# Kernel optimization log

Hardware: AMD Instinct MI355X
Metric: run time of the kernel (lower is better)

Reference implementation:

```python
import jax, jax.numpy as jnp
import numpy as np

B, S, D = 1, 4096, 2048
H, KVH, HD = 16, 4, 128  # heads, kv heads, head_dim
ROPE_BASE = 10000.0


def _rope_cos_sin(position_ids):
    # inv_freq: [HD/2]
    inv_freq = 1.0 / (ROPE_BASE ** (jnp.arange(0, HD, 2, dtype=jnp.float32) / HD))
    # freqs: [B, S, HD/2] -> emb: [B, S, HD] (concat(freqs, freqs))
    freqs = position_ids.astype(jnp.float32)[..., None] * inv_freq
    emb = jnp.concatenate([freqs, freqs], axis=-1)
    # [B, 1, S, HD] to broadcast over heads
    return jnp.cos(emb)[:, None, :, :], jnp.sin(emb)[:, None, :, :]


def _rotate_half(x):
    x1, x2 = x[..., : HD // 2], x[..., HD // 2 :]
    return jnp.concatenate([-x2, x1], axis=-1)


def setup_inputs() -> dict:
    key = jax.random.key(0)
    ks = jax.random.split(key, 5)
    s = 0.02
    return {
        "hidden_states": jax.random.normal(ks[0], (B, S, D), jnp.float32),
        "Wq": jax.random.normal(ks[1], (H * HD, D), jnp.float32) * s,
        "Wk": jax.random.normal(ks[2], (KVH * HD, D), jnp.float32) * s,
        "Wv": jax.random.normal(ks[3], (KVH * HD, D), jnp.float32) * s,
        "Wo": jax.random.normal(ks[4], (D, H * HD), jnp.float32) * s,
        "position_ids": jnp.arange(S, dtype=jnp.int64 if jax.config.jax_enable_x64 else jnp.int32)[None, :].repeat(B, 0),
    }


def reference(hidden_states, Wq, Wk, Wv, Wo, position_ids):
    b, s, _ = hidden_states.shape
    # projections (no bias): [b, s, nheads*hd] -> [b, nh, s, hd]
    q = (hidden_states @ Wq.T).reshape(b, s, H, HD).transpose(0, 2, 1, 3)
    k = (hidden_states @ Wk.T).reshape(b, s, KVH, HD).transpose(0, 2, 1, 3)
    v = (hidden_states @ Wv.T).reshape(b, s, KVH, HD).transpose(0, 2, 1, 3)

    cos, sin = _rope_cos_sin(position_ids)  # [b,1,s,hd]
    q = q * cos + _rotate_half(q) * sin
    k = k * cos + _rotate_half(k) * sin

    # GQA: repeat kv heads (repeat_interleave along head dim)
    n_rep = H // KVH
    k = jnp.repeat(k, n_rep, axis=1)
    v = jnp.repeat(v, n_rep, axis=1)

    # eager quadratic attention with causal mask
    scores = jnp.einsum("bhqd,bhkd->bhqk", q, k) / jnp.sqrt(jnp.float32(HD))
    causal = jnp.tril(jnp.ones((s, s), dtype=bool))
    scores = jnp.where(causal[None, None], scores, jnp.finfo(scores.dtype).min)
    attn = jax.nn.softmax(scores, axis=-1)
    out = jnp.einsum("bhqk,bhkd->bhqd", attn, v)  # [b,h,s,hd]
    out = out.transpose(0, 2, 1, 3).reshape(b, s, H * HD)
    return out @ Wo.T
```

## Files before the change

### kernel.cpp

```cpp
#include <hip/hip_runtime.h>
#include <hip/hip_bf16.h>

constexpr int S   = 4096;
constexpr int D   = 2048;
constexpr int H   = 16;
constexpr int KVH = 4;
constexpr int HD  = 128;

using short8 = __attribute__((ext_vector_type(8))) short;
using f32x4  = __attribute__((ext_vector_type(4))) float;
using f32x16 = __attribute__((ext_vector_type(16))) float;

__device__ inline ushort f2bf(float f) {
  union { float f; unsigned u; } x{f};
  unsigned r = x.u + 0x7FFFu + ((x.u >> 16) & 1u);
  return (ushort)(r >> 16);
}
__device__ inline float bf2f(ushort h) {
  union { unsigned u; float f; } x{(unsigned)h << 16};
  return x.f;
}
__device__ inline unsigned pkbf(float a, float b) {
  union { float f; unsigned u; } xa{a}, xb{b};
  unsigned ra = xa.u + 0x7FFFu + ((xa.u >> 16) & 1u);
  unsigned rb = xb.u + 0x7FFFu + ((xb.u >> 16) & 1u);
#if __has_builtin(__builtin_amdgcn_perm)
  return __builtin_amdgcn_perm(rb, ra, 0x07060302u);
#else
  return (rb & 0xFFFF0000u) | (ra >> 16);
#endif
}
__device__ inline unsigned pkbf_t(float a, float b) {
  union { float f; unsigned u; } xa{a}, xb{b};
#if __has_builtin(__builtin_amdgcn_perm)
  return __builtin_amdgcn_perm(xb.u, xa.u, 0x07060302u);
#else
  return (xb.u & 0xFFFF0000u) | (xa.u >> 16);
#endif
}
__device__ inline float fast_exp2(float x) {
#if __has_builtin(__builtin_amdgcn_exp2f)
  return __builtin_amdgcn_exp2f(x);
#else
  return exp2f(x);
#endif
}

__device__ inline void async_copy16(const ushort* g, ushort* l) {
  __builtin_amdgcn_global_load_lds(
      (const __attribute__((address_space(1))) unsigned int*)g,
      (__attribute__((address_space(3))) unsigned int*)l, 16, 0, 0);
}

constexpr size_t N_HID = (size_t)S * D;
constexpr size_t N_WQ  = (size_t)(H * HD) * D;
constexpr size_t N_WKV = (size_t)(KVH * HD) * D;
constexpr size_t C1_ = N_HID;
constexpr size_t C2_ = C1_ + N_WQ;
constexpr size_t C3_ = C2_ + N_WKV;
constexpr size_t C4_ = C3_ + N_WKV;
constexpr size_t C5_ = C4_ + N_WQ;

__global__ void cvt_all_kernel(const float* __restrict__ hid, const float* __restrict__ wq,
                               const float* __restrict__ wk, const float* __restrict__ wv,
                               const float* __restrict__ wo, ushort* __restrict__ dst) {
  size_t i = (size_t)blockIdx.x * blockDim.x + threadIdx.x;
  size_t off = i * 4;
  if (off >= C5_) return;
  const float* src;
  if      (off < C1_) src = hid + off;
  else if (off < C2_) src = wq + (off - C1_);
  else if (off < C3_) src = wk + (off - C2_);
  else if (off < C4_) src = wv + (off - C3_);
  else                src = wo + (off - C4_);
  float4 f = *(const float4*)src;
  ushort4 o;
  o.x = f2bf(f.x); o.y = f2bf(f.y); o.z = f2bf(f.z); o.w = f2bf(f.w);
  *(ushort4*)&dst[off] = o;
}

template <int OUT_MODE>
__device__ __forceinline__ void gemm_tile(const ushort* __restrict__ A,
                                          const ushort* __restrict__ Bt,
                                          void* __restrict__ Cv,
                                          int M, int N, int K, int bxi, int byi,
                                          ushort* As, ushort* Bs) {
  const int bm = byi * 128;
  const int bn = bxi * 128;
  const int tid  = threadIdx.x;
  const int lane = tid & 63;
  const int w    = tid >> 6;
  const int wr = w >> 1, wc = w & 1;
  const int lm = lane & 15, quad = lane >> 4;

  f32x4 acc[4][4];
#pragma unroll
  for (int i = 0; i < 4; ++i)
#pragma unroll
    for (int j = 0; j < 4; ++j) acc[i][j] = (f32x4){0.f, 0.f, 0.f, 0.f};

  for (int k0 = 0; k0 < K; k0 += 32) {
#pragma unroll
    for (int j = 0; j < 2; ++j) {
      int idx = j * 256 + tid;
      int row = idx >> 2;
      int col = (idx & 3) * 8;
      int ubase = (j * 256 + w * 64) * 8;
      async_copy16(A + (size_t)(bm + row) * K + k0 + col, &As[ubase]);
      async_copy16(Bt + (size_t)(bn + row) * K + k0 + col, &Bs[ubase]);
    }
    __syncthreads();
    short8 af[4], bfr[4];
#pragma unroll
    for (int t = 0; t < 4; ++t) {
      af[t]  = *(const short8*)&As[(wr * 64 + t * 16 + lm) * 32 + quad * 8];
      bfr[t] = *(const short8*)&Bs[(wc * 64 + t * 16 + lm) * 32 + quad * 8];
    }
#pragma unroll
    for (int i = 0; i < 4; ++i)
#pragma unroll
      for (int j = 0; j < 4; ++j)
        acc[i][j] = __builtin_amdgcn_mfma_f32_16x16x32_bf16(af[i], bfr[j], acc[i][j], 0, 0, 0);
    __syncthreads();
  }

#pragma unroll
  for (int i = 0; i < 4; ++i)
#pragma unroll
    for (int j = 0; j < 4; ++j) {
      if (OUT_MODE == 2) {
        int col  = bn + wc * 64 + j * 16 + lm;
        int rowb = bm + wr * 64 + i * 16 + quad * 4;
        ushort4 o4;
        o4.x = f2bf(acc[i][j][0]); o4.y = f2bf(acc[i][j][1]);
        o4.z = f2bf(acc[i][j][2]); o4.w = f2bf(acc[i][j][3]);
        *(ushort4*)&((ushort*)Cv)[(size_t)col * M + rowb] = o4;
      } else {
#pragma unroll
        for (int r = 0; r < 4; ++r) {
          size_t row = bm + wr * 64 + i * 16 + quad * 4 + r;
          size_t col = bn + wc * 64 + j * 16 + lm;
          if (OUT_MODE == 1) ((ushort*)Cv)[row * N + col] = f2bf(acc[i][j][r]);
          else               ((float*)Cv)[row * N + col]  = acc[i][j][r];
        }
      }
    }
}

__global__ __launch_bounds__(256) void gemm_qkv_kernel(const ushort* __restrict__ hb,
                                                       const ushort* __restrict__ wq,
                                                       const ushort* __restrict__ wk,
                                                       const ushort* __restrict__ wv,
                                                       ushort* __restrict__ qb,
                                                       ushort* __restrict__ kb,
                                                       ushort* __restrict__ vtb) {
  __shared__ __align__(16) ushort As[128 * 32];
  __shared__ __align__(16) ushort Bs[128 * 32];
  int bid = blockIdx.x;
  if (bid < 512) {
    gemm_tile<1>(hb, wq, qb, S, H * HD, D, bid & 15, bid >> 4, As, Bs);
  } else if (bid < 640) {
    int b = bid - 512;
    gemm_tile<1>(hb, wk, kb, S, KVH * HD, D, b & 3, b >> 2, As, Bs);
  } else {
    int b = bid - 640;
    gemm_tile<2>(hb, wv, vtb, S, KVH * HD, D, b & 3, b >> 2, As, Bs);
  }
}

template <int OUT_MODE>
__global__ __launch_bounds__(256) void gemm_bt_kernel(const ushort* __restrict__ A,
                                                      const ushort* __restrict__ Bt,
                                                      void* __restrict__ Cv,
                                                      int M, int N, int K) {
  __shared__ __align__(16) ushort As[128 * 32];
  __shared__ __align__(16) ushort Bs[128 * 32];
  gemm_tile<OUT_MODE>(A, Bt, Cv, M, N, K, blockIdx.x, blockIdx.y, As, Bs);
}

__global__ void rope_bf16_kernel(ushort* __restrict__ qb, ushort* __restrict__ kb,
                                 const int* __restrict__ pos_ids) {
  int idx = blockIdx.x * blockDim.x + threadIdx.x;
  const int total = S * (H + KVH) * (HD / 2);
  if (idx >= total) return;
  int j = idx & 63;
  int t = idx >> 6;
  int head = t % (H + KVH);
  int s = t / (H + KVH);
  float p = (float)pos_ids[s];
  float inv_freq = exp2f(-(float)j * (13.287712379549449f / 64.0f));
  float ang = p * inv_freq;
  float c = cosf(ang), sn = sinf(ang);
  ushort* base = (head < H) ? (qb + (size_t)s * (H * HD) + head * HD)
                            : (kb + (size_t)s * (KVH * HD) + (head - H) * HD);
  float x1 = bf2f(base[j]), x2 = bf2f(base[j + 64]);
  base[j]      = f2bf(x1 * c - x2 * sn);
  base[j + 64] = f2bf(x2 * c + x1 * sn);
}

__global__ __launch_bounds__(512) void attn_mfma_kernel(const ushort* __restrict__ q,
                                                        const ushort* __restrict__ k,
                                                        const ushort* __restrict__ Vt,
                                                        ushort* __restrict__ o) {
  const int bid = blockIdx.x;
  const int h   = 2 * (bid & 7) + ((bid >> 3) & 1);
  const int t   = bid >> 4;
  const int qi  = 31 - t;
  const int q0  = qi * 128;
  const int kvh = h >> 2;
  const int tid  = threadIdx.x;
  const int lane = tid & 63;
  const int w    = tid >> 6;
  const int qw   = w >> 1;
  const int ks   = w & 1;
  const int m32  = lane & 31;
  const int p    = lane >> 5;

  __shared__ __align__(16) ushort LDSu[32768];

  const int q0w = q0 + qw * 32;

  short8 qf[8];
#pragma unroll
  for (int s = 0; s < 8; ++s)
    qf[s] = *(const short8*)&q[(size_t)(q0w + m32) * (H * HD) + h * HD + s * 16 + p * 8];

  f32x16 Oacc[4];
#pragma unroll
  for (int i = 0; i < 4; ++i)
#pragma unroll
    for (int r = 0; r < 16; ++r) Oacc[i][r] = 0.f;
  float ls4[4] = {0.f, 0.f, 0.f, 0.f};

  auto stage = [&](int k0s, int buf) {
#pragma unroll
    for (int i = 0; i < 4; ++i) {
      int c = w * 4 + i;
      if (c < 16) {
        int kh = c >> 3, s = c & 7;
        async_copy16(&k[(size_t)(k0s + kh * 32 + m32) * (KVH * HD) + kvh * HD + s * 16 + p * 8],
                     &LDSu[buf * 8192 + c * 512]);
      } else {
        int cv = c - 16;
        int ht = cv >> 2, t2 = cv & 3;
        async_copy16(&Vt[(size_t)(kvh * HD + ht * 32 + m32) * S + k0s + t2 * 16 + p * 8],
                     &LDSu[16384 + buf * 8192 + cv * 512]);
      }
    }
  };

  stage(0, 0);
  __syncthreads();

  const float C1  = 0.08838834764831845f * 1.4426950408889634f;
  const float F2n = -12.0f * 1.4426950408889634f;
  const int T = 2 * qi + 2;

  for (int tt = 0; tt < T; ++tt) {
    const int k0  = tt * 64;
    const int cur = tt & 1;
    if (tt + 1 < T) stage(k0 + 64, cur ^ 1);
    const ushort* Kb = &LDSu[cur * 8192];
    const ushort* Vb = &LDSu[16384 + cur * 8192];

    const int kbase = k0 + ks * 32;
    if (kbase <= q0w + 31) {
      f32x16 stA, stB;
#pragma unroll
      for (int r = 0; r < 16; ++r) { stA[r] = 0.f; stB[r] = 0.f; }
#pragma unroll
      for (int s = 0; s < 8; s += 2) {
        short8 kf0 = *(const short8*)&Kb[(ks * 8 + s) * 512 + lane * 8];
        short8 kf1 = *(const short8*)&Kb[(ks * 8 + s + 1) * 512 + lane * 8];
        stA = __builtin_amdgcn_mfma_f32_32x32x16_bf16(kf0, qf[s], stA, 0, 0, 0);
        stB = __builtin_amdgcn_mfma_f32_32x32x16_bf16(kf1, qf[s + 1], stB, 0, 0, 0);
      }

      float pv[16];
      if (kbase == q0w) {
#pragma unroll
        for (int r = 0; r < 16; ++r) {
          int kvl = (r & 3) + 8 * (r >> 2) + 4 * p;
          float e = fast_exp2(fmaf(stA[r] + stB[r], C1, F2n));
          e = (kvl > m32) ? 0.f : e;
          pv[r] = e; ls4[r & 3] += e;
        }
      } else {
#pragma unroll
        for (int r = 0; r < 16; ++r) {
          float e = fast_exp2(fmaf(stA[r] + stB[r], C1, F2n));
          pv[r] = e; ls4[r & 3] += e;
        }
      }

      unsigned own2[4][2], oth[4][2];
#pragma unroll
      for (int g = 0; g < 4; ++g) {
        own2[g][0] = pkbf_t(pv[4 * g + 0], pv[4 * g + 1]);
        own2[g][1] = pkbf_t(pv[4 * g + 2], pv[4 * g + 3]);
        oth[g][0]  = __shfl_xor(own2[g][0], 32);
        oth[g][1]  = __shfl_xor(own2[g][1], 32);
      }
      short8 pf[2];
#pragma unroll
      for (int t2 = 0; t2 < 2; ++t2) {
        union { unsigned u4[4]; short8 s8; } pb;
        pb.u4[0] = p ? oth[2 * t2 + 1][0] : own2[2 * t2][0];
        pb.u4[1] = p ? oth[2 * t2 + 1][1] : own2[2 * t2][1];
        pb.u4[2] = p ? own2[2 * t2 + 1][0] : oth[2 * t2][0];
        pb.u4[3] = p ? own2[2 * t2 + 1][1] : oth[2 * t2][1];
        pf[t2] = pb.s8;
      }

#pragma unroll
      for (int ht = 0; ht < 4; ++ht)
#pragma unroll
        for (int t2l = 0; t2l < 2; ++t2l) {
          int cv = ht * 4 + ks * 2 + t2l;
          short8 vf = *(const short8*)&Vb[cv * 512 + lane * 8];
          Oacc[ht] = __builtin_amdgcn_mfma_f32_32x32x16_bf16(vf, pf[t2l], Oacc[ht], 0, 0, 0);
        }
    }
    __syncthreads();
  }

  float lsum = (ls4[0] + ls4[1]) + (ls4[2] + ls4[3]);
  float* mb = (float*)LDSu;

  if (ks) mb[(qw << 6) | lane] = lsum;
  __syncthreads();
  if (!ks) lsum += mb[(qw << 6) | lane];
  __syncthreads();

  if (ks) {
    float* base = mb + qw * 4096;
#pragma unroll
    for (int ht = 0; ht < 4; ++ht)
#pragma unroll
      for (int r = 0; r < 16; ++r)
        base[ht * 1024 + r * 64 + lane] = Oacc[ht][r];
  }
  __syncthreads();

  if (!ks) {
    const float* base = mb + qw * 4096;
#pragma unroll
    for (int ht = 0; ht < 4; ++ht)
#pragma unroll
      for (int r = 0; r < 16; ++r)
        Oacc[ht][r] += base[ht * 1024 + r * 64 + lane];

    float ltot = lsum + __shfl_xor(lsum, 32);
    float inv = 1.0f / ltot;
#pragma unroll
    for (int ht = 0; ht < 4; ++ht)
#pragma unroll
      for (int rq = 0; rq < 4; ++rq) {
        uint2 dd;
        dd.x = pkbf(Oacc[ht][4 * rq + 0] * inv, Oacc[ht][4 * rq + 1] * inv);
        dd.y = pkbf(Oacc[ht][4 * rq + 2] * inv, Oacc[ht][4 * rq + 3] * inv);
        *(uint2*)&o[(size_t)(q0w + m32) * (H * HD) + h * HD + ht * 32 + 8 * rq + 4 * p] = dd;
      }
  }
}

extern "C" void kernel_launch(void* const* d_in, const int* in_sizes, int n_in,
                              void* d_out, int out_size, void* d_ws, size_t ws_size,
                              hipStream_t stream) {
  const float* hidden = (const float*)d_in[0];
  const float* Wq     = (const float*)d_in[1];
  const float* Wk     = (const float*)d_in[2];
  const float* Wv     = (const float*)d_in[3];
  const float* Wo     = (const float*)d_in[4];
  const int*   pos    = (const int*)d_in[5];
  float* out = (float*)d_out;

  ushort* hb  = (ushort*)d_ws;
  ushort* wqb = hb  + N_HID;
  ushort* wkb = wqb + N_WQ;
  ushort* wvb = wkb + N_WKV;
  ushort* wob = wvb + N_WKV;
  ushort* qb  = wob + N_WQ;
  ushort* kb  = qb  + (size_t)S * (H * HD);
  ushort* vtb = kb  + (size_t)S * (KVH * HD);
  ushort* ob  = vtb + (size_t)(KVH * HD) * S;

  dim3 blk(256);
  size_t n4 = C5_ / 4;
  cvt_all_kernel<<<(int)((n4 + 255) / 256), blk, 0, stream>>>(hidden, Wq, Wk, Wv, Wo, hb);

  gemm_qkv_kernel<<<dim3(768), blk, 0, stream>>>(hb, wqb, wkb, wvb, qb, kb, vtb);

  int rope_total = S * (H + KVH) * (HD / 2);
  rope_bf16_kernel<<<(rope_total + 255) / 256, blk, 0, stream>>>(qb, kb, pos);

  attn_mfma_kernel<<<dim3(512), dim3(512), 0, stream>>>(qb, kb, vtb, ob);

  gemm_bt_kernel<0><<<dim3(D / 128, S / 128), blk, 0, stream>>>(ob, wob, out, S, D, D);
}
```

Measured before the change: 353.4 us.

## Load V fragments directly from global and halve attention LDS footprint

V tiles are no longer staged through LDS. Each wave reads its V^T MFMA fragments straight from global memory, which halves the shared buffer from 64KB to 32KB, and the final cross-wave Oacc reduction is split into two passes so it fits. The P fragment exchange between half-waves uses permlane32_swap when the compiler provides it, replacing two shuffles plus selects. Intent is higher occupancy and fewer LDS round trips and shuffles, at the cost of exposed global-load latency for V inside the inner loop.

```diff
diff --git a/kernel.cpp b/kernel.cpp
--- a/kernel.cpp
+++ b/kernel.cpp
@@ -43,6 +43,19 @@
   return __builtin_amdgcn_exp2f(x);
 #else
   return exp2f(x);
+#endif
+}
+
+__device__ inline void swap_half(unsigned a, unsigned b, unsigned& x, unsigned& y) {
+#if __has_builtin(__builtin_amdgcn_permlane32_swap)
+  using uint2v = __attribute__((ext_vector_type(2))) unsigned;
+  uint2v r = __builtin_amdgcn_permlane32_swap(a, b, false, false);
+  x = r[0]; y = r[1];
+#else
+  unsigned bx = __shfl_xor(b, 32), ax = __shfl_xor(a, 32);
+  int p = (threadIdx.x & 63) >> 5;
+  x = p ? bx : a;
+  y = p ? b : ax;
 #endif
 }
 
@@ -216,7 +229,7 @@
   const int m32  = lane & 31;
   const int p    = lane >> 5;
 
-  __shared__ __align__(16) ushort LDSu[32768];
+  __shared__ __align__(16) ushort LDSu[16384];
 
   const int q0w = q0 + qw * 32;
 
@@ -234,18 +247,11 @@
 
   auto stage = [&](int k0s, int buf) {
 #pragma unroll
-    for (int i = 0; i < 4; ++i) {
-      int c = w * 4 + i;
-      if (c < 16) {
-        int kh = c >> 3, s = c & 7;
-        async_copy16(&k[(size_t)(k0s + kh * 32 + m32) * (KVH * HD) + kvh * HD + s * 16 + p * 8],
-                     &LDSu[buf * 8192 + c * 512]);
-      } else {
-        int cv = c - 16;
-        int ht = cv >> 2, t2 = cv & 3;
-        async_copy16(&Vt[(size_t)(kvh * HD + ht * 32 + m32) * S + k0s + t2 * 16 + p * 8],
-                     &LDSu[16384 + buf * 8192 + cv * 512]);
-      }
+    for (int i = 0; i < 2; ++i) {
+      int c = w * 2 + i;
+      int kh = c >> 3, s = c & 7;
+      async_copy16(&k[(size_t)(k0s + kh * 32 + m32) * (KVH * HD) + kvh * HD + s * 16 + p * 8],
+                   &LDSu[buf * 8192 + c * 512]);
     }
   };
 
@@ -261,10 +267,11 @@
     const int cur = tt & 1;
     if (tt + 1 < T) stage(k0 + 64, cur ^ 1);
     const ushort* Kb = &LDSu[cur * 8192];
-    const ushort* Vb = &LDSu[16384 + cur * 8192];
 
     const int kbase = k0 + ks * 32;
     if (kbase <= q0w + 31) {
+      const ushort* vg = &Vt[(size_t)(kvh * HD + m32) * S + k0 + ks * 32 + p * 8];
+
       f32x16 stA, stB;
 #pragma unroll
       for (int r = 0; r < 16; ++r) { stA[r] = 0.f; stB[r] = 0.f; }
@@ -293,22 +300,20 @@
         }
       }
 
-      unsigned own2[4][2], oth[4][2];
+      unsigned own2[4][2];
 #pragma unroll
       for (int g = 0; g < 4; ++g) {
         own2[g][0] = pkbf_t(pv[4 * g + 0], pv[4 * g + 1]);
         own2[g][1] = pkbf_t(pv[4 * g + 2], pv[4 * g + 3]);
-        oth[g][0]  = __shfl_xor(own2[g][0], 32);
-        oth[g][1]  = __shfl_xor(own2[g][1], 32);
       }
       short8 pf[2];
 #pragma unroll
       for (int t2 = 0; t2 < 2; ++t2) {
+        unsigned x0, y0, x1, y1;
+        swap_half(own2[2 * t2][0], own2[2 * t2 + 1][0], x0, y0);
+        swap_half(own2[2 * t2][1], own2[2 * t2 + 1][1], x1, y1);
         union { unsigned u4[4]; short8 s8; } pb;
-        pb.u4[0] = p ? oth[2 * t2 + 1][0] : own2[2 * t2][0];
-        pb.u4[1] = p ? oth[2 * t2 + 1][1] : own2[2 * t2][1];
-        pb.u4[2] = p ? own2[2 * t2 + 1][0] : oth[2 * t2][0];
-        pb.u4[3] = p ? own2[2 * t2 + 1][1] : oth[2 * t2][1];
+        pb.u4[0] = x0; pb.u4[1] = x1; pb.u4[2] = y0; pb.u4[3] = y1;
         pf[t2] = pb.s8;
       }
 
@@ -316,8 +321,7 @@
       for (int ht = 0; ht < 4; ++ht)
 #pragma unroll
         for (int t2l = 0; t2l < 2; ++t2l) {
-          int cv = ht * 4 + ks * 2 + t2l;
-          short8 vf = *(const short8*)&Vb[cv * 512 + lane * 8];
+          short8 vf = *(const short8*)(vg + (size_t)(ht * 32) * S + t2l * 16);
           Oacc[ht] = __builtin_amdgcn_mfma_f32_32x32x16_bf16(vf, pf[t2l], Oacc[ht], 0, 0, 0);
         }
     }
@@ -332,24 +336,27 @@
   if (!ks) lsum += mb[(qw << 6) | lane];
   __syncthreads();
 
-  if (ks) {
-    float* base = mb + qw * 4096;
-#pragma unroll
-    for (int ht = 0; ht < 4; ++ht)
-#pragma unroll
-      for (int r = 0; r < 16; ++r)
-        base[ht * 1024 + r * 64 + lane] = Oacc[ht][r];
+#pragma unroll
+  for (int hh = 0; hh < 2; ++hh) {
+    if (ks) {
+#pragma unroll
+      for (int hq = 0; hq < 2; ++hq)
+#pragma unroll
+        for (int r = 0; r < 16; ++r)
+          mb[((qw * 2 + hq) * 16 + r) * 64 + lane] = Oacc[hh * 2 + hq][r];
+    }
+    __syncthreads();
+    if (!ks) {
+#pragma unroll
+      for (int hq = 0; hq < 2; ++hq)
+#pragma unroll
+        for (int r = 0; r < 16; ++r)
+          Oacc[hh * 2 + hq][r] += mb[((qw * 2 + hq) * 16 + r) * 64 + lane];
+    }
+    __syncthreads();
   }
-  __syncthreads();
 
   if (!ks) {
-    const float* base = mb + qw * 4096;
-#pragma unroll
-    for (int ht = 0; ht < 4; ++ht)
-#pragma unroll
-      for (int r = 0; r < 16; ++r)
-        Oacc[ht][r] += base[ht * 1024 + r * 64 + lane];
-
     float ltot = lsum + __shfl_xor(lsum, 32);
     float inv = 1.0f / ltot;
 #pragma unroll
```

After: 443.0 us. 25.3% more time.

## Double-buffer GEMM LDS tiles and use permlane32 swap for P fragment exchange

Applied to the files above, without the earlier changes.

The GEMM tile loop now uses two LDS buffers, issuing async global-to-LDS loads for the next K slice before computing the current one, so load latency can overlap with MFMA work. Separately, the attention kernel's P-fragment exchange between wave halves replaces eight shfl_xor (ds_bpermute) calls plus selects with permlane32_swap when that builtin exists. LDS use for the GEMMs doubles, which may reduce occupancy. The single barrier per iteration relies on the async loads landing and on the buffer being fully read before it is overwritten, which risks a race.

```diff
diff --git a/kernel.cpp b/kernel.cpp
--- a/kernel.cpp
+++ b/kernel.cpp
@@ -43,6 +43,19 @@
   return __builtin_amdgcn_exp2f(x);
 #else
   return exp2f(x);
+#endif
+}
+
+__device__ inline void swap_half(unsigned a, unsigned b, unsigned& x, unsigned& y) {
+#if __has_builtin(__builtin_amdgcn_permlane32_swap)
+  using uint2v = __attribute__((ext_vector_type(2))) unsigned;
+  uint2v r = __builtin_amdgcn_permlane32_swap(a, b, false, false);
+  x = r[0]; y = r[1];
+#else
+  unsigned bx = __shfl_xor(b, 32), ax = __shfl_xor(a, 32);
+  int p = (threadIdx.x & 63) >> 5;
+  x = p ? bx : a;
+  y = p ? b : ax;
 #endif
 }
 
@@ -99,22 +112,31 @@
 #pragma unroll
     for (int j = 0; j < 4; ++j) acc[i][j] = (f32x4){0.f, 0.f, 0.f, 0.f};
 
-  for (int k0 = 0; k0 < K; k0 += 32) {
+  auto stage = [&](int k0, int buf) {
 #pragma unroll
     for (int j = 0; j < 2; ++j) {
       int idx = j * 256 + tid;
       int row = idx >> 2;
       int col = (idx & 3) * 8;
-      int ubase = (j * 256 + w * 64) * 8;
+      int ubase = buf * 4096 + (j * 256 + w * 64) * 8;
       async_copy16(A + (size_t)(bm + row) * K + k0 + col, &As[ubase]);
       async_copy16(Bt + (size_t)(bn + row) * K + k0 + col, &Bs[ubase]);
     }
-    __syncthreads();
+  };
+
+  stage(0, 0);
+  __syncthreads();
+
+  for (int k0 = 0; k0 < K; k0 += 32) {
+    const int cur = (k0 >> 5) & 1;
+    if (k0 + 32 < K) stage(k0 + 32, cur ^ 1);
+    const ushort* Ac = As + cur * 4096;
+    const ushort* Bc = Bs + cur * 4096;
     short8 af[4], bfr[4];
 #pragma unroll
     for (int t = 0; t < 4; ++t) {
-      af[t]  = *(const short8*)&As[(wr * 64 + t * 16 + lm) * 32 + quad * 8];
-      bfr[t] = *(const short8*)&Bs[(wc * 64 + t * 16 + lm) * 32 + quad * 8];
+      af[t]  = *(const short8*)&Ac[(wr * 64 + t * 16 + lm) * 32 + quad * 8];
+      bfr[t] = *(const short8*)&Bc[(wc * 64 + t * 16 + lm) * 32 + quad * 8];
     }
 #pragma unroll
     for (int i = 0; i < 4; ++i)
@@ -154,8 +176,8 @@
                                                        ushort* __restrict__ qb,
                                                        ushort* __restrict__ kb,
                                                        ushort* __restrict__ vtb) {
-  __shared__ __align__(16) ushort As[128 * 32];
-  __shared__ __align__(16) ushort Bs[128 * 32];
+  __shared__ __align__(16) ushort As[2 * 128 * 32];
+  __shared__ __align__(16) ushort Bs[2 * 128 * 32];
   int bid = blockIdx.x;
   if (bid < 512) {
     gemm_tile<1>(hb, wq, qb, S, H * HD, D, bid & 15, bid >> 4, As, Bs);
@@ -173,8 +195,8 @@
                                                       const ushort* __restrict__ Bt,
                                                       void* __restrict__ Cv,
                                                       int M, int N, int K) {
-  __shared__ __align__(16) ushort As[128 * 32];
-  __shared__ __align__(16) ushort Bs[128 * 32];
+  __shared__ __align__(16) ushort As[2 * 128 * 32];
+  __shared__ __align__(16) ushort Bs[2 * 128 * 32];
   gemm_tile<OUT_MODE>(A, Bt, Cv, M, N, K, blockIdx.x, blockIdx.y, As, Bs);
 }
 
@@ -293,22 +315,20 @@
         }
       }
 
-      unsigned own2[4][2], oth[4][2];
+      unsigned own2[4][2];
 #pragma unroll
       for (int g = 0; g < 4; ++g) {
         own2[g][0] = pkbf_t(pv[4 * g + 0], pv[4 * g + 1]);
         own2[g][1] = pkbf_t(pv[4 * g + 2], pv[4 * g + 3]);
-        oth[g][0]  = __shfl_xor(own2[g][0], 32);
-        oth[g][1]  = __shfl_xor(own2[g][1], 32);
       }
       short8 pf[2];
 #pragma unroll
       for (int t2 = 0; t2 < 2; ++t2) {
+        unsigned x0, y0, x1, y1;
+        swap_half(own2[2 * t2][0], own2[2 * t2 + 1][0], x0, y0);
+        swap_half(own2[2 * t2][1], own2[2 * t2 + 1][1], x1, y1);
         union { unsigned u4[4]; short8 s8; } pb;
-        pb.u4[0] = p ? oth[2 * t2 + 1][0] : own2[2 * t2][0];
-        pb.u4[1] = p ? oth[2 * t2 + 1][1] : own2[2 * t2][1];
-        pb.u4[2] = p ? own2[2 * t2 + 1][0] : oth[2 * t2][0];
-        pb.u4[3] = p ? own2[2 * t2 + 1][1] : oth[2 * t2][1];
+        pb.u4[0] = x0; pb.u4[1] = x1; pb.u4[2] = y0; pb.u4[3] = y1;
         pf[t2] = pb.s8;
       }
 
```

Result: slower. 365.6 us (+3.4%).
